# Optimization experiments

Measured on AMD Instinct MI355X. Metric: run time of the kernel, lower is better.

Reference implementation:

```python
import jax, jax.numpy as jnp
import numpy as np

EPS = 1e-5


def _conv1x1(h, w, b):
    # 1x1 conv == per-pixel matmul: (b,c,h,w) x (o,c) -> (b,o,h,w)
    return jnp.einsum('bchw,oc->bohw', h, w) + b[None, :, None, None]


def setup_inputs() -> dict:
    key = jax.random.key(0)
    ks = jax.random.split(key, 7)
    B, C, H, W = 4, 512, 64, 64
    s = 0.02
    return {
        'x': jax.random.normal(ks[0], (B, C, H, W), dtype=jnp.float32),
        'wq': jax.random.normal(ks[1], (C, C), dtype=jnp.float32) * s,
        'bq': jax.random.normal(ks[2], (C,), dtype=jnp.float32) * s,
        'wk': jax.random.normal(ks[3], (C, C), dtype=jnp.float32) * s,
        'bk': jax.random.normal(ks[4], (C,), dtype=jnp.float32) * s,
        'wv': jax.random.normal(ks[5], (C, C), dtype=jnp.float32) * s,
        'bv': jax.random.normal(ks[6], (C,), dtype=jnp.float32) * s,
    }


def reference(x, wq, bq, wk, bk, wv, bv):
    B, C, H, W = x.shape
    # InstanceNorm2d (affine=False): normalize over spatial dims per (b, c)
    mu = jnp.mean(x, axis=(2, 3), keepdims=True)
    var = jnp.var(x, axis=(2, 3), keepdims=True)  # biased, matches torch
    h_ = (x - mu) * jax.lax.rsqrt(var + EPS)

    q = _conv1x1(h_, wq, bq).reshape(B, C, H * W)  # (b, c, n)
    k = _conv1x1(h_, wk, bk).reshape(B, C, H * W)
    v = _conv1x1(h_, wv, bv).reshape(B, C, H * W)

    scale = float(int(C)) ** (-0.5)
    attn = jnp.einsum('bcq,bck->bqk', q, k) * scale  # (b, n_q, n_k)
    attn = jax.nn.softmax(attn, axis=-1)
    # torch: bmm(v, attn.permute(0,2,1)) -> A[b,c,q] = sum_k v[b,c,k] * attn[b,q,k]
    A = jnp.einsum('bck,bqk->bcq', v, attn).reshape(B, C, H, W)
    return x + A
```

## Files before the change

### kernel.cpp

```cpp
#include <hip/hip_runtime.h>
#include <hip/hip_bf16.h>
#include <cstdint>

#define B_ 4
#define C_ 512
#define N_ 4096

typedef unsigned short u16;
typedef unsigned char u8;
typedef __bf16 bf16x8 __attribute__((ext_vector_type(8)));
typedef float f32x4 __attribute__((ext_vector_type(4)));

union U16B { uint4 u; bf16x8 v; };

__device__ __forceinline__ bf16x8 ld16g(const u16* p) {
  U16B t; t.u = *(const uint4*)p; return t.v;
}

__device__ __forceinline__ u16 f2bf(float f) {
  uint32_t u = __builtin_bit_cast(uint32_t, f);
  u = (u + 0x7FFFu + ((u >> 16) & 1u)) >> 16;
  return (u16)u;
}
__device__ __forceinline__ float bf2f(u16 h) {
  uint32_t u = ((uint32_t)h) << 16;
  return __builtin_bit_cast(float, u);
}

__device__ __forceinline__ u8 f2fp8(float f) {
  uint32_t u = __builtin_bit_cast(uint32_t, f);
  uint32_t s = (u >> 24) & 0x80u;
  uint32_t a = u & 0x7FFFFFFFu;
  if (a >= 0x43700000u) return (u8)(s | 0x7E);
  if (a < 0x3C800000u) {
    float af = __builtin_bit_cast(float, a);
    int m = (int)(af * 512.0f + 0.5f);
    return (u8)(s | (uint32_t)m);
  }
  uint32_t r = (a + 0x7FFFFu + ((a >> 20) & 1u)) >> 20;
  return (u8)(s | (r - (120u << 3)));
}

__device__ __forceinline__ u8 f2bf8pos(float f) {
  _Float16 h = (_Float16)f;
  u16 hb = __builtin_bit_cast(unsigned short, h);
  hb = (u16)(hb + 0x7Fu + ((hb >> 8) & 1u));
  return (u8)(hb >> 8);
}

typedef const __attribute__((address_space(1))) uint32_t* gas_p;
typedef __attribute__((address_space(3))) uint32_t* las_p;
__device__ __forceinline__ void gld16(const void* g, void* l) {
  __builtin_amdgcn_global_load_lds((gas_p)g, (las_p)l, 16, 0, 0);
}

#define SCEXP 0.06376149809794171f

__global__ __launch_bounds__(256) void cvt_w(const float* __restrict__ w, u16* __restrict__ o) {
  int i = blockIdx.x * 256 + threadIdx.x;
  float4 v = ((const float4*)w)[i];
  ushort4 r;
  r.x = f2bf(v.x); r.y = f2bf(v.y); r.z = f2bf(v.z); r.w = f2bf(v.w);
  ((ushort4*)o)[i] = r;
}

__global__ __launch_bounds__(256) void prep_wb(
    const float* __restrict__ wq, const float* __restrict__ wk,
    const float* __restrict__ wv, const float* __restrict__ bq,
    const float* __restrict__ bk, u8* __restrict__ wqk8,
    u8* __restrict__ wv8, float* __restrict__ bqk)
{
  int blk = blockIdx.x, t = threadIdx.x;
  if (blk < 768) {
    const float* src = blk < 256 ? wq : (blk < 512 ? wk : wv);
    u8* dst = blk < 256 ? wqk8 : (blk < 512 ? wqk8 + 262144 : wv8);
    int i = (blk & 255) * 256 + t;
    float4 v = ((const float4*)src)[i];
    uchar4 r;
    r.x = f2fp8(v.x); r.y = f2fp8(v.y); r.z = f2fp8(v.z); r.w = f2fp8(v.w);
    ((uchar4*)dst)[i] = r;
  } else {
#pragma unroll
    for (int j = 0; j < 4; ++j) {
      int i = j * 256 + t;
      bqk[i] = (i < 512) ? bq[i] : bk[i - 512];
    }
  }
}

__global__ __launch_bounds__(256) void inorm_stats(const float* __restrict__ x,
    float* __restrict__ mu, float* __restrict__ rstd) {
  int bc = blockIdx.x;
  const float4* p = (const float4*)(x + (size_t)bc * N_);
  float s = 0.f, ss = 0.f;
  for (int i = threadIdx.x; i < N_ / 4; i += 256) {
    float4 v = p[i];
    s  += v.x + v.y + v.z + v.w;
    ss += v.x * v.x + v.y * v.y + v.z * v.z + v.w * v.w;
  }
#pragma unroll
  for (int off = 32; off > 0; off >>= 1) {
    s  += __shfl_down(s, off);
    ss += __shfl_down(ss, off);
  }
  __shared__ float as_[4], ass_[4];
  if ((threadIdx.x & 63) == 0) { as_[threadIdx.x >> 6] = s; ass_[threadIdx.x >> 6] = ss; }
  __syncthreads();
  if (threadIdx.x == 0) {
    float S  = as_[0] + as_[1] + as_[2] + as_[3];
    float SS = ass_[0] + ass_[1] + ass_[2] + ass_[3];
    float m  = S * (1.f / N_);
    float var = SS * (1.f / N_) - m * m;
    mu[bc] = m;
    rstd[bc] = rsqrtf(var + 1e-5f);
  }
}

__global__ __launch_bounds__(256) void norm_h8(const float* __restrict__ x,
    const float* __restrict__ mu, const float* __restrict__ rstd, u8* __restrict__ h8) {
  __shared__ u16 tile[128][66];
  int b = blockIdx.z, c0 = blockIdx.y * 128, n0 = blockIdx.x * 64;
  int t = threadIdx.x;
  const float* xb = x + ((size_t)b * C_ + c0) * N_ + n0;
#pragma unroll
  for (int it = 0; it < 32; ++it) {
    int idx = it * 256 + t;
    int row = idx >> 6, n = idx & 63;
    float m  = mu[b * C_ + c0 + row];
    float rs = rstd[b * C_ + c0 + row];
    tile[row][n] = f2bf((xb[(size_t)row * N_ + n] - m) * rs);
  }
  __syncthreads();
  u8* ob = h8 + ((size_t)b * N_ + n0) * C_ + c0;
#pragma unroll
  for (int it = 0; it < 32; ++it) {
    int idx = it * 256 + t;
    int n = idx >> 7, c = idx & 127;
    ob[(size_t)n * C_ + c] = f2fp8(bf2f(tile[c][n]));
  }
}

__global__ __launch_bounds__(256) void norm_transpose(const float* __restrict__ x,
    const float* __restrict__ mu, const float* __restrict__ rstd, u16* __restrict__ hT) {
  __shared__ u16 tile[64][66];
  int b = blockIdx.z, c0 = blockIdx.y * 64, n0 = blockIdx.x * 64;
  int tn = threadIdx.x & 63, t4 = threadIdx.x >> 6;
  const float* xb = x + ((size_t)b * C_ + c0) * N_ + n0;
#pragma unroll
  for (int it = 0; it < 16; ++it) {
    int c = t4 + it * 4;
    float m  = mu[b * C_ + c0 + c];
    float rs = rstd[b * C_ + c0 + c];
    tile[c][tn] = f2bf((xb[(size_t)c * N_ + tn] - m) * rs);
  }
  __syncthreads();
  u16* hTb = hT + ((size_t)b * N_ + n0) * C_ + c0;
#pragma unroll
  for (int it = 0; it < 16; ++it) {
    int n = t4 + it * 4;
    hTb[(size_t)n * C_ + tn] = tile[tn][n];
  }
}

#define EPI_Q 0
#define EPI_V 1

template<int EPI>
__global__ __launch_bounds__(512, 3) void proj8(
    const u8* __restrict__ A, const u8* __restrict__ B,
    const float* __restrict__ aux, u8* __restrict__ Out,
    long sAz, long sBz, long sOz, int ldo)
{
  int z = blockIdx.z;
  const u8* Ab = A + (size_t)z * sAz;
  const u8* Bb = B + (size_t)z * sBz;
  u8* ob = Out + (size_t)z * sOz;
  int m0 = blockIdx.x * 128, n0 = blockIdx.y * 256;

  int t = threadIdx.x, w = t >> 6, l = t & 63;
  int wr = w >> 2, wc = w & 3;
  int l16 = l & 15, lg = l >> 4;

  __shared__ char smem[49152];

  f32x4 acc[4][4] = {};
  int rg = ((lg ^ ((l16 >> 1) & 3)) & 3) << 4;

#define STGJ(step, lb) {                                                     \
    size_t kb = (size_t)(step) * 64;                                         \
    {                                                                        \
      int row = t >> 2, g = t & 3;                                           \
      int sg = (g ^ ((row >> 1) & 3)) << 4;                                  \
      gld16((const char*)Ab + (size_t)(m0 + row) * 512 + kb + sg,            \
            (lb) + (size_t)t * 16);                                          \
    }                                                                        \
    _Pragma("unroll")                                                        \
    for (int i = 0; i < 2; ++i) {                                            \
      int s2 = i * 512 + t;                                                  \
      int row = s2 >> 2, g = s2 & 3;                                         \
      int sg = (g ^ ((row >> 1) & 3)) << 4;                                  \
      gld16((const char*)Bb + (size_t)(n0 + row) * 512 + kb + sg,            \
            (lb) + 8192 + (size_t)s2 * 16);                                  \
    }                                                                        \
  }

#define COMPJ(lb) {                                                          \
    const char* Al = (lb);                                                   \
    const char* Bl = (lb) + 8192;                                            \
    uint4 af[4], bf[4];                                                      \
    _Pragma("unroll")                                                        \
    for (int mf = 0; mf < 4; ++mf)                                           \
      af[mf] = *(const uint4*)(Al + (wr * 64 + mf * 16 + l16) * 64 + rg);    \
    _Pragma("unroll")                                                        \
    for (int nf = 0; nf < 4; ++nf)                                           \
      bf[nf] = *(const uint4*)(Bl + (wc * 64 + nf * 16 + l16) * 64 + rg);    \
    _Pragma("unroll")                                                        \
    for (int kk = 0; kk < 2; ++kk) {                                         \
      _Pragma("unroll")                                                      \
      for (int mf = 0; mf < 4; ++mf) {                                       \
        long long a8 = ((long long)(kk ? af[mf].w : af[mf].y) << 32) |       \
                       (unsigned int)(kk ? af[mf].z : af[mf].x);             \
        _Pragma("unroll")                                                    \
        for (int nf = 0; nf < 4; ++nf) {                                     \
          long long b8 = ((long long)(kk ? bf[nf].w : bf[nf].y) << 32) |     \
                         (unsigned int)(kk ? bf[nf].z : bf[nf].x);           \
          acc[mf][nf] = __builtin_amdgcn_mfma_f32_16x16x32_fp8_fp8(          \
              a8, b8, acc[mf][nf], 0, 0, 0);                                 \
        }                                                                    \
      }                                                                      \
    }                                                                        \
  }

  char* buf0 = smem;
  char* buf1 = smem + 24576;

  STGJ(0, buf0);
#pragma unroll
  for (int s = 0; s < 8; ++s) {
    char* cb = (s & 1) ? buf1 : buf0;
    char* nb = (s & 1) ? buf0 : buf1;
    if (s < 7) {
      STGJ(s + 1, nb);
      asm volatile("s_waitcnt vmcnt(3)" ::: "memory");
    } else {
      asm volatile("s_waitcnt vmcnt(0)" ::: "memory");
    }
    __builtin_amdgcn_s_barrier();
    __builtin_amdgcn_sched_barrier(0);
    COMPJ(cb);
    __builtin_amdgcn_sched_barrier(0);
    __builtin_amdgcn_s_barrier();
  }
#undef STGJ
#undef COMPJ

  if constexpr (EPI == EPI_Q) {
    float bc[4];
#pragma unroll
    for (int nf = 0; nf < 4; ++nf) bc[nf] = aux[n0 + wc * 64 + nf * 16 + l16];
#pragma unroll
    for (int mf = 0; mf < 4; ++mf) {
#pragma unroll
      for (int r = 0; r < 4; ++r) {
        int row = wr * 64 + mf * 16 + lg * 4 + r;
        int gx = ((row >> 2) & 3) << 4;
#pragma unroll
        for (int nf = 0; nf < 4; ++nf) {
          int cl = wc * 64 + nf * 16 + l16;
          smem[row * 256 + (cl ^ gx)] = (char)f2fp8(acc[mf][nf][r] + bc[nf]);
        }
      }
    }
    __syncthreads();
#pragma unroll
    for (int it = 0; it < 4; ++it) {
      int idx = it * 512 + t;
      int row = idx >> 4, seg = idx & 15;
      int gx = ((row >> 2) & 3) << 4;
      uint4 v = *(const uint4*)(smem + row * 256 + ((seg * 16) ^ gx));
      *(uint4*)(ob + (size_t)(m0 + row) * ldo + n0 + seg * 16) = v;
    }
  } else {
#pragma unroll
    for (int mf = 0; mf < 4; ++mf) {
#pragma unroll
      for (int r = 0; r < 4; ++r) {
        int row = wr * 64 + mf * 16 + lg * 4 + r;
        float brow = aux[m0 + row];
        uint32_t pk = 0;
#pragma unroll
        for (int nf = 0; nf < 4; ++nf)
          pk |= (uint32_t)f2fp8(acc[mf][nf][r] + brow) << (8 * nf);
        int blk = (wc ^ lg) << 6;
        *(uint32_t*)(smem + row * 256 + blk + l16 * 4) = pk;
      }
    }
    __syncthreads();
#pragma unroll
    for (int it = 0; it < 4; ++it) {
      int idx = it * 512 + t;
      int row = idx >> 4, seg = idx & 15;
      int blk = ((seg >> 2) ^ ((row >> 2) & 3)) << 6;
      uint4 v = *(const uint4*)(smem + row * 256 + blk + (seg & 3) * 16);
      *(uint4*)(ob + (size_t)(m0 + row) * ldo + n0 + seg * 16) = v;
    }
  }
}

__global__ __launch_bounds__(512, 3) void exp8(
    const u8* __restrict__ qk8, float* __restrict__ dsumAll, u8* __restrict__ Pall)
{
  int fid = blockIdx.x;
  int rid = (fid & 7) * 256 + (fid >> 3);
  int z = rid >> 9;
  int r9 = rid & 511;
  int c2 = r9 >> 8;
  int r8 = r9 & 255;
  int sm = r8 >> 6, w6s = r8 & 63;
  int m0 = (c2 * 16 + (sm >> 1) * 8 + (w6s >> 3)) * 128;
  int n0 = ((sm & 1) * 8 + (w6s & 7)) * 256;

  const u8* Ab = qk8 + (size_t)z * ((size_t)N_ * 1024);
  const u8* Bb = Ab + 512;
  float* dsum = dsumAll + (size_t)z * N_;
  u8* Pp = Pall + (size_t)z * (size_t)N_ * N_;

  int t = threadIdx.x, w = t >> 6, l = t & 63;
  int wr = w >> 2, wc = w & 3;
  int l16 = l & 15, lg = l >> 4;

  __shared__ char smem[49152];

  f32x4 acc[4][4] = {};
  int rg = ((lg ^ ((l16 >> 1) & 3)) & 3) << 4;

#define STG8(step, lb) {                                                     \
    size_t kb = (size_t)(step) * 64;                                         \
    {                                                                        \
      int row = t >> 2, g = t & 3;                                           \
      int sg = (g ^ ((row >> 1) & 3)) << 4;                                  \
      gld16((const char*)Ab + (size_t)(m0 + row) * 1024 + kb + sg,           \
            (lb) + (size_t)t * 16);                                          \
    }                                                                        \
    _Pragma("unroll")                                                        \
    for (int i = 0; i < 2; ++i) {                                            \
      int s2 = i * 512 + t;                                                  \
      int row = s2 >> 2, g = s2 & 3;                                         \
      int sg = (g ^ ((row >> 1) & 3)) << 4;                                  \
      gld16((const char*)Bb + (size_t)(n0 + row) * 1024 + kb + sg,           \
            (lb) + 8192 + (size_t)s2 * 16);                                  \
    }                                                                        \
  }

#define COMP8(lb) {                                                          \
    const char* Al = (lb);                                                   \
    const char* Bl = (lb) + 8192;                                            \
    uint4 af[4], bf[4];                                                      \
    _Pragma("unroll")                                                        \
    for (int mf = 0; mf < 4; ++mf)                                           \
      af[mf] = *(const uint4*)(Al + (wr * 64 + mf * 16 + l16) * 64 + rg);    \
    _Pragma("unroll")                                                        \
    for (int nf = 0; nf < 4; ++nf)                                           \
      bf[nf] = *(const uint4*)(Bl + (wc * 64 + nf * 16 + l16) * 64 + rg);    \
    _Pragma("unroll")                                                        \
    for (int kk = 0; kk < 2; ++kk) {                                         \
      _Pragma("unroll")                                                      \
      for (int mf = 0; mf < 4; ++mf) {                                       \
        long long a8 = ((long long)(kk ? af[mf].w : af[mf].y) << 32) |       \
                       (unsigned int)(kk ? af[mf].z : af[mf].x);             \
        _Pragma("unroll")                                                    \
        for (int nf = 0; nf < 4; ++nf) {                                     \
          long long b8 = ((long long)(kk ? bf[nf].w : bf[nf].y) << 32) |     \
                         (unsigned int)(kk ? bf[nf].z : bf[nf].x);           \
          acc[mf][nf] = __builtin_amdgcn_mfma_f32_16x16x32_fp8_fp8(          \
              a8, b8, acc[mf][nf], 0, 0, 0);                                 \
        }                                                                    \
      }                                                                      \
    }                                                                        \
  }

  char* buf0 = smem;
  char* buf1 = smem + 24576;

  STG8(0, buf0);
#pragma unroll
  for (int s = 0; s < 8; ++s) {
    char* cb = (s & 1) ? buf1 : buf0;
    char* nb = (s & 1) ? buf0 : buf1;
    if (s < 7) {
      STG8(s + 1, nb);
      asm volatile("s_waitcnt vmcnt(3)" ::: "memory");
    } else {
      asm volatile("s_waitcnt vmcnt(0)" ::: "memory");
    }
    __builtin_amdgcn_s_barrier();
    __builtin_amdgcn_sched_barrier(0);
    COMP8(cb);
    __builtin_amdgcn_sched_barrier(0);
    __builtin_amdgcn_s_barrier();
  }
#undef STG8
#undef COMP8

#pragma unroll
  for (int mf = 0; mf < 4; ++mf) {
#pragma unroll
    for (int r = 0; r < 4; ++r) {
      int row = wr * 64 + mf * 16 + lg * 4 + r;
      float rs = 0.f;
      uint32_t pk = 0;
#pragma unroll
      for (int nf = 0; nf < 4; ++nf) {
        float p = __builtin_amdgcn_exp2f(acc[mf][nf][r] * SCEXP);
        rs += p;
        pk |= (uint32_t)f2bf8pos(p) << (8 * nf);
      }
      int blk = (wc ^ lg) << 6;
      *(uint32_t*)(smem + row * 256 + blk + l16 * 4) = pk;
      rs += __shfl_xor(rs, 1); rs += __shfl_xor(rs, 2);
      rs += __shfl_xor(rs, 4); rs += __shfl_xor(rs, 8);
      if (l16 == 0) atomicAdd(&dsum[m0 + row], rs);
    }
  }
  __syncthreads();
#pragma unroll
  for (int it = 0; it < 4; ++it) {
    int idx = it * 512 + t;
    int row = idx >> 4, seg = idx & 15;
    int blk = ((seg >> 2) ^ ((row >> 2) & 3)) << 6;
    *(uint4*)(Pp + ((size_t)(m0 + row) * N_ + n0 + seg * 16)) =
        *(const uint4*)(smem + row * 256 + blk + (seg & 3) * 16);
  }
}

__global__ __launch_bounds__(256, 4) void pv8(
    const u8* __restrict__ vM8, const u8* __restrict__ P8,
    const float* __restrict__ denom, const float* __restrict__ x,
    float* __restrict__ out)
{
  int fid = blockIdx.x;
  int rid = (fid & 7) * 64 + (fid >> 3);
  int z = rid >> 7;
  int r7 = rid & 127;
  int n0 = (r7 >> 2) * 128;
  int m0 = (r7 & 3) * 128;

  const u8* Ab = vM8 + (size_t)z * ((size_t)C_ * N_);
  const u8* Bb = P8 + (size_t)z * ((size_t)N_ * N_);
  const float* db = denom + (size_t)z * N_;
  const float* xb = x + (size_t)z * ((size_t)C_ * N_);
  float* ob = out + (size_t)z * ((size_t)C_ * N_);

  int t = threadIdx.x, w = t >> 6, l = t & 63;
  int wr = w >> 1, wc = w & 1;
  int l16 = l & 15, lg = l >> 4;

  __shared__ char smem[32768];

  f32x4 acc[4][4] = {};
  int rg = ((lg ^ ((l16 >> 1) & 3)) & 3) << 4;

#define STGP(step, lb) {                                                     \
    size_t kb = (size_t)(step) * 64;                                         \
    _Pragma("unroll")                                                        \
    for (int i = 0; i < 2; ++i) {                                            \
      int s2 = i * 256 + t;                                                  \
      int row = s2 >> 2, g = s2 & 3;                                         \
      int sg = (g ^ ((row >> 1) & 3)) << 4;                                  \
      gld16((const char*)Ab + (size_t)(m0 + row) * N_ + kb + sg,             \
            (lb) + (size_t)s2 * 16);                                         \
      gld16((const char*)Bb + (size_t)(n0 + row) * N_ + kb + sg,             \
            (lb) + 8192 + (size_t)s2 * 16);                                  \
    }                                                                        \
  }

#define COMPP(lb) {                                                          \
    const char* Al = (lb);                                                   \
    const char* Bl = (lb) + 8192;                                            \
    uint4 af[4], bf[4];                                                      \
    _Pragma("unroll")                                                        \
    for (int mf = 0; mf < 4; ++mf)                                           \
      af[mf] = *(const uint4*)(Al + (wr * 64 + mf * 16 + l16) * 64 + rg);    \
    _Pragma("unroll")                                                        \
    for (int nf = 0; nf < 4; ++nf)                                           \
      bf[nf] = *(const uint4*)(Bl + (wc * 64 + nf * 16 + l16) * 64 + rg);    \
    _Pragma("unroll")                                                        \
    for (int kk = 0; kk < 2; ++kk) {                                         \
      _Pragma("unroll")                                                      \
      for (int mf = 0; mf < 4; ++mf) {                                       \
        long long a8 = ((long long)(kk ? af[mf].w : af[mf].y) << 32) |       \
                       (unsigned int)(kk ? af[mf].z : af[mf].x);             \
        _Pragma("unroll")                                                    \
        for (int nf = 0; nf < 4; ++nf) {                                     \
          long long b8 = ((long long)(kk ? bf[nf].w : bf[nf].y) << 32) |     \
                         (unsigned int)(kk ? bf[nf].z : bf[nf].x);           \
          acc[mf][nf] = __builtin_amdgcn_mfma_f32_16x16x32_fp8_bf8(          \
              a8, b8, acc[mf][nf], 0, 0, 0);                                 \
        }                                                                    \
      }                                                                      \
    }                                                                        \
  }

  char* buf0 = smem;
  char* buf1 = smem + 16384;

  STGP(0, buf0);
#pragma unroll 2
  for (int s = 0; s < 64; ++s) {
    char* cb = (s & 1) ? buf1 : buf0;
    char* nb = (s & 1) ? buf0 : buf1;
    if (s < 63) {
      STGP(s + 1, nb);
      asm volatile("s_waitcnt vmcnt(4)" ::: "memory");
    } else {
      asm volatile("s_waitcnt vmcnt(0)" ::: "memory");
    }
    __builtin_amdgcn_s_barrier();
    __builtin_amdgcn_sched_barrier(0);
    COMPP(cb);
    __builtin_amdgcn_sched_barrier(0);
    __builtin_amdgcn_s_barrier();
  }
#undef STGP
#undef COMPP

  float rd[4];
#pragma unroll
  for (int nf = 0; nf < 4; ++nf)
    rd[nf] = 1.0f / db[n0 + wc * 64 + nf * 16 + l16];
#pragma unroll
  for (int mf = 0; mf < 4; ++mf) {
#pragma unroll
    for (int r = 0; r < 4; ++r) {
      int row = m0 + wr * 64 + mf * 16 + lg * 4 + r;
#pragma unroll
      for (int nf = 0; nf < 4; ++nf) {
        int col = n0 + wc * 64 + nf * 16 + l16;
        size_t o = (size_t)row * N_ + col;
        ob[o] = xb[o] + acc[mf][nf][r] * rd[nf];
      }
    }
  }
}

__global__ __launch_bounds__(256) void gemm_abT(
    const u16* __restrict__ A, const u16* __restrict__ Bm,
    const float* __restrict__ bias, u16* __restrict__ out,
    int ldo, int bias_is_row)
{
  int w = threadIdx.x >> 6, l = threadIdx.x & 63;
  int l16 = l & 15, lg = l >> 4;
  int m0 = blockIdx.x * 128 + (w >> 1) * 64;
  int n0 = blockIdx.y * 128 + (w & 1) * 64;
  f32x4 acc[4][4] = {};
  const u16* Ab = A  + (size_t)(m0 + l16) * 512 + lg * 8;
  const u16* Bb = Bm + (size_t)(n0 + l16) * 512 + lg * 8;
  for (int kc = 0; kc < 512; kc += 32) {
    bf16x8 af[4], bf[4];
#pragma unroll
    for (int i = 0; i < 4; ++i) af[i] = ld16g(Ab + (size_t)(i * 16) * 512 + kc);
#pragma unroll
    for (int j = 0; j < 4; ++j) bf[j] = ld16g(Bb + (size_t)(j * 16) * 512 + kc);
#pragma unroll
    for (int i = 0; i < 4; ++i)
#pragma unroll
      for (int j = 0; j < 4; ++j)
        acc[i][j] = __builtin_amdgcn_mfma_f32_16x16x32_bf16(af[i], bf[j], acc[i][j], 0, 0, 0);
  }
#pragma unroll
  for (int i = 0; i < 4; ++i) {
#pragma unroll
    for (int j = 0; j < 4; ++j) {
      int col = n0 + j * 16 + l16;
#pragma unroll
      for (int r = 0; r < 4; ++r) {
        int row = m0 + i * 16 + lg * 4 + r;
        float v = acc[i][j][r] + (bias_is_row ? bias[row] : bias[col]);
        out[(size_t)row * ldo + col] = f2bf(v);
      }
    }
  }
}

#define NQ 32
#define NKB 64
__global__ __launch_bounds__(512) void attn_kernel(
    const u16* __restrict__ qT, const u16* __restrict__ kT, const u16* __restrict__ vM,
    const float* __restrict__ x, float* __restrict__ out)
{
  int b = blockIdx.y;
  int nq0 = blockIdx.x * NQ;
  const u16* qTb = qT + (size_t)b * N_ * C_;
  const u16* kTb = kT + (size_t)b * N_ * C_;
  const u16* vb  = vM + (size_t)b * C_ * N_;
  const float* xb = x + (size_t)b * C_ * N_;
  float* ob = out + (size_t)b * C_ * N_;

  int tid = threadIdx.x;
  int w = tid >> 6, l = tid & 63, l16 = l & 15, lg = l >> 4;
  int nqf = w & 1, nkf = w >> 1;
  int c0 = w * 64;

  __shared__ u16 qlds[32][520];
  __shared__ u16 Plds[32][72];
  __shared__ float dpart[32][16];
  __shared__ float dfin[32];

  for (int idx = tid; idx < 32 * 64; idx += 512) {
    int row = idx >> 6, cg = idx & 63;
    *(uint4*)&qlds[row][cg * 8] = *(const uint4*)(qTb + (size_t)(nq0 + row) * C_ + cg * 8);
  }
  __syncthreads();

  f32x4 acc[2][4] = {};
  float dreg = 0.f;
  int drow = tid >> 4, dcol = (tid & 15) * 4;

  for (int nk0 = 0; nk0 < N_; nk0 += NKB) {
    f32x4 s = {0.f, 0.f, 0.f, 0.f};
    const u16* krow = kTb + (size_t)(nk0 + nkf * 16 + l16) * C_ + lg * 8;
#pragma unroll 4
    for (int kc = 0; kc < 16; ++kc) {
      U16B tq; tq.u = *(const uint4*)&qlds[nqf * 16 + l16][kc * 32 + lg * 8];
      bf16x8 kf = ld16g(krow + kc * 32);
      s = __builtin_amdgcn_mfma_f32_16x16x32_bf16(tq.v, kf, s, 0, 0, 0);
    }
    __syncthreads();
#pragma unroll
    for (int r = 0; r < 4; ++r) {
      float p = __builtin_amdgcn_exp2f(s[r] * SCEXP);
      Plds[nqf * 16 + lg * 4 + r][nkf * 16 + l16] = f2bf(p);
    }
    __syncthreads();
#pragma unroll
    for (int r = 0; r < 4; ++r) dreg += bf2f(Plds[drow][dcol + r]);
#pragma unroll
    for (int kk = 0; kk < 2; ++kk) {
      bf16x8 pf[2];
#pragma unroll
      for (int i = 0; i < 2; ++i) {
        U16B t2; t2.u = *(const uint4*)&Plds[i * 16 + l16][kk * 32 + lg * 8];
        pf[i] = t2.v;
      }
#pragma unroll
      for (int j = 0; j < 4; ++j) {
        bf16x8 vf = ld16g(vb + (size_t)(c0 + j * 16 + l16) * N_ + nk0 + kk * 32 + lg * 8);
#pragma unroll
        for (int i = 0; i < 2; ++i)
          acc[i][j] = __builtin_amdgcn_mfma_f32_16x16x32_bf16(pf[i], vf, acc[i][j], 0, 0, 0);
      }
    }
  }

  dpart[drow][tid & 15] = dreg;
  __syncthreads();
  if (tid < 32) {
    float s2 = 0.f;
#pragma unroll
    for (int g = 0; g < 16; ++g) s2 += dpart[tid][g];
    dfin[tid] = s2;
  }
  __syncthreads();

#pragma unroll
  for (int i = 0; i < 2; ++i) {
    float dinv[4];
#pragma unroll
    for (int r = 0; r < 4; ++r) dinv[r] = 1.f / dfin[i * 16 + lg * 4 + r];
    int nbase = nq0 + i * 16 + lg * 4;
#pragma unroll
    for (int j = 0; j < 4; ++j) {
      int c = c0 + j * 16 + l16;
      float4 xv = *(const float4*)(xb + (size_t)c * N_ + nbase);
      float4 o;
      o.x = xv.x + acc[i][j][0] * dinv[0];
      o.y = xv.y + acc[i][j][1] * dinv[1];
      o.z = xv.z + acc[i][j][2] * dinv[2];
      o.w = xv.w + acc[i][j][3] * dinv[3];
      *(float4*)(ob + (size_t)c * N_ + nbase) = o;
    }
  }
}

extern "C" void kernel_launch(void* const* d_in, const int* in_sizes, int n_in,
                              void* d_out, int out_size, void* d_ws, size_t ws_size,
                              hipStream_t stream) {
  (void)in_sizes; (void)n_in; (void)out_size;
  const float* x  = (const float*)d_in[0];
  const float* wq = (const float*)d_in[1];
  const float* bq = (const float*)d_in[2];
  const float* wk = (const float*)d_in[3];
  const float* bk = (const float*)d_in[4];
  const float* wv = (const float*)d_in[5];
  const float* bv = (const float*)d_in[6];
  float* out = (float*)d_out;
  char* ws = (char*)d_ws;

  const size_t NC = (size_t)N_ * C_;
  const size_t NEED = 101535744;

  if (ws_size >= NEED) {
    u8*    wqk8  = (u8*)(ws);
    u8*    wv8   = (u8*)(ws + 524288);
    float* bqk   = (float*)(ws + 786432);
    float* mu    = (float*)(ws + 790528);
    float* rstd  = (float*)(ws + 798720);
    u8*    h8    = (u8*)(ws + 806912);
    u8*    qk8   = (u8*)(ws + 9195520);
    u8*    vM8   = (u8*)(ws + 25972736);
    float* denom = (float*)(ws + 34361344);
    u8*    P8    = (u8*)(ws + 34426880);

    prep_wb<<<769, 256, 0, stream>>>(wq, wk, wv, bq, bk, wqk8, wv8, bqk);
    inorm_stats<<<B_ * C_, 256, 0, stream>>>(x, mu, rstd);
    norm_h8<<<dim3(N_ / 64, C_ / 128, B_), 256, 0, stream>>>(x, mu, rstd, h8);
    hipMemsetAsync(denom, 0, 4 * N_ * sizeof(float), stream);

    proj8<EPI_Q><<<dim3(32, 4, 4), 512, 0, stream>>>(
        h8, wqk8, bqk, qk8, (long)NC, 0, (long)N_ * 1024, 1024);
    proj8<EPI_V><<<dim3(4, 16, 4), 512, 0, stream>>>(
        wv8, h8, bv, vM8, 0, (long)NC, (long)NC, 4096);

    exp8<<<2048, 512, 0, stream>>>(qk8, denom, P8);

    pv8<<<512, 256, 0, stream>>>(vM8, P8, denom, x, out);
  } else {
    u16*   wbf_q = (u16*)(ws);
    u16*   wbf_k = (u16*)(ws + 524288);
    u16*   wbf_v = (u16*)(ws + 1048576);
    float* mu    = (float*)(ws + 1572864);
    float* rstd  = (float*)(ws + 1581056);
    u16*   hT    = (u16*)(ws + 1589248);
    u16*   qT    = (u16*)(ws + 18366464);
    u16*   kT    = (u16*)(ws + 35143680);
    u16*   vM    = (u16*)(ws + 51920896);

    cvt_w<<<256, 256, 0, stream>>>(wq, wbf_q);
    cvt_w<<<256, 256, 0, stream>>>(wk, wbf_k);
    cvt_w<<<256, 256, 0, stream>>>(wv, wbf_v);
    inorm_stats<<<B_ * C_, 256, 0, stream>>>(x, mu, rstd);
    norm_transpose<<<dim3(N_ / 64, C_ / 64, B_), 256, 0, stream>>>(x, mu, rstd, hT);

    for (int b = 0; b < B_; ++b) {
      const u16* hTb = hT + (size_t)b * NC;
      u16* qTb = qT + (size_t)b * NC;
      u16* kTb = kT + (size_t)b * NC;
      u16* vMb = vM + (size_t)b * NC;
      gemm_abT<<<dim3(N_ / 128, C_ / 128), 256, 0, stream>>>(hTb, wbf_q, bq, qTb, C_, 0);
      gemm_abT<<<dim3(N_ / 128, C_ / 128), 256, 0, stream>>>(hTb, wbf_k, bk, kTb, C_, 0);
      gemm_abT<<<dim3(C_ / 128, N_ / 128), 256, 0, stream>>>(wbf_v, hTb, bv, vMb, N_, 1);
    }
    attn_kernel<<<dim3(N_ / NQ, B_), 512, 0, stream>>>(qT, kT, vM, x, out);
  }
}
```

Measured before the change: 220.4 us.

## Make exp8 blocks persistent over four column tiles with in-loop epilogue

The exp8 kernel now launches 512 blocks instead of 2048. Each block walks four consecutive 256-wide column tiles of the QK^T matrix for a fixed 128-row stripe, running an exp/pack/store epilogue every 8 k-steps and then resetting the accumulators. This cuts launch and tail overhead, keeps the A stripe hot in cache, and pipelines the next tile's loads across tile boundaries. In exchange the epilogue reuses the current LDS buffer in two halves with extra barriers, and there are fewer blocks to fill the GPU.

```diff
diff --git a/kernel.cpp b/kernel.cpp
--- a/kernel.cpp
+++ b/kernel.cpp
@@ -311,14 +311,11 @@
     const u8* __restrict__ qk8, float* __restrict__ dsumAll, u8* __restrict__ Pall)
 {
   int fid = blockIdx.x;
-  int rid = (fid & 7) * 256 + (fid >> 3);
-  int z = rid >> 9;
-  int r9 = rid & 511;
-  int c2 = r9 >> 8;
-  int r8 = r9 & 255;
-  int sm = r8 >> 6, w6s = r8 & 63;
-  int m0 = (c2 * 16 + (sm >> 1) * 8 + (w6s >> 3)) * 128;
-  int n0 = ((sm & 1) * 8 + (w6s & 7)) * 256;
+  int rid = (fid & 7) * 64 + (fid >> 3);
+  int z = rid >> 7;
+  int r7 = rid & 127;
+  int m0 = (r7 >> 2) * 128;
+  int nbase = (r7 & 3) * 1024;
 
   const u8* Ab = qk8 + (size_t)z * ((size_t)N_ * 1024);
   const u8* Bb = Ab + 512;
@@ -334,8 +331,9 @@
   f32x4 acc[4][4] = {};
   int rg = ((lg ^ ((l16 >> 1) & 3)) & 3) << 4;
 
-#define STG8(step, lb) {                                                     \
-    size_t kb = (size_t)(step) * 64;                                         \
+#define STG8(ph, lb) {                                                       \
+    size_t kb = (size_t)((ph) & 7) * 64;                                     \
+    int n0p = nbase + ((ph) >> 3) * 256;                                     \
     {                                                                        \
       int row = t >> 2, g = t & 3;                                           \
       int sg = (g ^ ((row >> 1) & 3)) << 4;                                  \
@@ -347,7 +345,7 @@
       int s2 = i * 512 + t;                                                  \
       int row = s2 >> 2, g = s2 & 3;                                         \
       int sg = (g ^ ((row >> 1) & 3)) << 4;                                  \
-      gld16((const char*)Bb + (size_t)(n0 + row) * 1024 + kb + sg,           \
+      gld16((const char*)Bb + (size_t)(n0p + row) * 1024 + kb + sg,          \
             (lb) + 8192 + (size_t)s2 * 16);                                  \
     }                                                                        \
   }
@@ -383,12 +381,12 @@
   char* buf1 = smem + 24576;
 
   STG8(0, buf0);
-#pragma unroll
-  for (int s = 0; s < 8; ++s) {
-    char* cb = (s & 1) ? buf1 : buf0;
-    char* nb = (s & 1) ? buf0 : buf1;
-    if (s < 7) {
-      STG8(s + 1, nb);
+#pragma unroll 2
+  for (int p = 0; p < 32; ++p) {
+    char* cb = (p & 1) ? buf1 : buf0;
+    char* nb = (p & 1) ? buf0 : buf1;
+    if (p < 31) {
+      STG8(p + 1, nb);
       asm volatile("s_waitcnt vmcnt(3)" ::: "memory");
     } else {
       asm volatile("s_waitcnt vmcnt(0)" ::: "memory");
@@ -398,39 +396,53 @@
     COMP8(cb);
     __builtin_amdgcn_sched_barrier(0);
     __builtin_amdgcn_s_barrier();
+    if ((p & 7) == 7) {
+      int n0t = nbase + (p >> 3) * 256;
+#pragma unroll
+      for (int h = 0; h < 2; ++h) {
+        if ((wc >> 1) == h) {
+#pragma unroll
+          for (int mf = 0; mf < 4; ++mf) {
+#pragma unroll
+            for (int r = 0; r < 4; ++r) {
+              int row = wr * 64 + mf * 16 + lg * 4 + r;
+              float rs = 0.f;
+              uint32_t pk = 0;
+#pragma unroll
+              for (int nf = 0; nf < 4; ++nf) {
+                float pv = __builtin_amdgcn_exp2f(acc[mf][nf][r] * SCEXP);
+                rs += pv;
+                pk |= (uint32_t)f2bf8pos(pv) << (8 * nf);
+              }
+              int blk = ((wc & 1) ^ ((row >> 2) & 1)) << 6;
+              *(uint32_t*)(cb + row * 128 + blk + l16 * 4) = pk;
+              rs += __shfl_xor(rs, 1); rs += __shfl_xor(rs, 2);
+              rs += __shfl_xor(rs, 4); rs += __shfl_xor(rs, 8);
+              if (l16 == 0) atomicAdd(&dsum[m0 + row], rs);
+            }
+          }
+        }
+        __builtin_amdgcn_s_barrier();
+#pragma unroll
+        for (int it = 0; it < 2; ++it) {
+          int idx = it * 512 + t;
+          int row = idx >> 3, seg = idx & 7;
+          int blkr = ((seg >> 2) ^ ((row >> 2) & 1)) << 6;
+          *(uint4*)(Pp + ((size_t)(m0 + row) * N_ + n0t + h * 128 +
+                          (seg >> 2) * 64 + (seg & 3) * 16)) =
+              *(const uint4*)(cb + row * 128 + blkr + (seg & 3) * 16);
+        }
+        __builtin_amdgcn_s_barrier();
+      }
+#pragma unroll
+      for (int mf = 0; mf < 4; ++mf)
+#pragma unroll
+        for (int nf = 0; nf < 4; ++nf)
+          acc[mf][nf] = f32x4{0.f, 0.f, 0.f, 0.f};
+    }
   }
 #undef STG8
 #undef COMP8
-
-#pragma unroll
-  for (int mf = 0; mf < 4; ++mf) {
-#pragma unroll
-    for (int r = 0; r < 4; ++r) {
-      int row = wr * 64 + mf * 16 + lg * 4 + r;
-      float rs = 0.f;
-      uint32_t pk = 0;
-#pragma unroll
-      for (int nf = 0; nf < 4; ++nf) {
-        float p = __builtin_amdgcn_exp2f(acc[mf][nf][r] * SCEXP);
-        rs += p;
-        pk |= (uint32_t)f2bf8pos(p) << (8 * nf);
-      }
-      int blk = (wc ^ lg) << 6;
-      *(uint32_t*)(smem + row * 256 + blk + l16 * 4) = pk;
-      rs += __shfl_xor(rs, 1); rs += __shfl_xor(rs, 2);
-      rs += __shfl_xor(rs, 4); rs += __shfl_xor(rs, 8);
-      if (l16 == 0) atomicAdd(&dsum[m0 + row], rs);
-    }
-  }
-  __syncthreads();
-#pragma unroll
-  for (int it = 0; it < 4; ++it) {
-    int idx = it * 512 + t;
-    int row = idx >> 4, seg = idx & 15;
-    int blk = ((seg >> 2) ^ ((row >> 2) & 3)) << 6;
-    *(uint4*)(Pp + ((size_t)(m0 + row) * N_ + n0 + seg * 16)) =
-        *(const uint4*)(smem + row * 256 + blk + (seg & 3) * 16);
-  }
 }
 
 __global__ __launch_bounds__(256, 4) void pv8(
@@ -721,7 +733,7 @@
     proj8<EPI_V><<<dim3(4, 16, 4), 512, 0, stream>>>(
         wv8, h8, bv, vM8, 0, (long)NC, (long)NC, 4096);
 
-    exp8<<<2048, 512, 0, stream>>>(qk8, denom, P8);
+    exp8<<<512, 512, 0, stream>>>(qk8, denom, P8);
 
     pv8<<<512, 256, 0, stream>>>(vM8, P8, denom, x, out);
   } else {
```

Result: slower. 253.7 us (+15.1%).
